# Kernel tuning notes

Measured on AMD Instinct MI355X. Metric: run time of the kernel, lower is better.

Reference implementation:

```python
import jax, jax.numpy as jnp
import numpy as np

B, N, D_IN = 8, 8192, 13
RATIO, R, K = 0.25, 0.2, 32


def setup_inputs() -> dict:
    key = jax.random.key(0)
    k1, k2, k3, k4 = jax.random.split(key, 4)
    x = jax.random.normal(k1, (B, N, D_IN), dtype=jnp.float32)
    pos = jax.random.uniform(k2, (B, N, 3), dtype=jnp.float32)
    batch = jnp.broadcast_to(jnp.arange(B, dtype=jnp.int32)[:, None], (B, N))
    W1 = jax.random.normal(k3, (D_IN + 3, 64), dtype=jnp.float32) * 0.1
    b1 = jnp.zeros((64,), jnp.float32)
    W2 = jax.random.normal(k4, (64, 128), dtype=jnp.float32) * 0.1
    b2 = jnp.zeros((128,), jnp.float32)
    return {"x": x, "pos": pos, "batch": batch, "W1": W1, "b1": b1, "W2": W2, "b2": b2}


def _fps_single(p, M):
    """Deterministic farthest point sampling (start at index 0). p: [N,3] -> [M] int32."""
    n = p.shape[0]

    def step(carry, _):
        mind, last = carry
        d = jnp.sum((p - p[last]) ** 2, axis=-1)
        mind = jnp.minimum(mind, d)
        nxt = jnp.argmax(mind).astype(jnp.int32)
        return (mind, nxt), nxt

    init = (jnp.full((n,), 1e10, p.dtype), jnp.int32(0))
    _, rest = jax.lax.scan(step, init, None, length=M - 1)
    return jnp.concatenate([jnp.zeros((1,), jnp.int32), rest])


def reference(x, pos, batch, W1, b1, W2, b2):
    M = int(RATIO * N)
    # --- FPS per cloud ---
    idx = jax.vmap(lambda p: _fps_single(p, M))(pos)              # [B, M]
    pos_s = jnp.take_along_axis(pos, idx[..., None], axis=1)      # [B, M, 3]
    # --- radius ball query: first K in-ball neighbors by point index ---
    d2 = jnp.sum((pos_s[:, :, None, :] - pos[:, None, :, :]) ** 2, axis=-1)  # [B, M, N]
    within = d2 <= R * R
    rank = jnp.where(within, jnp.arange(N, dtype=jnp.int32), N)   # invalid -> N
    negv, nbr = jax.lax.top_k(-rank, K)                           # K smallest ranks
    valid = negv > -N                                             # [B, M, K]
    # --- gather -> local_nn MLP -> masked max-scatter (PointNetConv) ---
    x_j = jax.vmap(lambda a, i: a[i])(x, nbr)                     # [B, M, K, D_IN]
    pos_j = jax.vmap(lambda a, i: a[i])(pos, nbr)                 # [B, M, K, 3]
    feat = jnp.concatenate([x_j, pos_j - pos_s[:, :, None, :]], axis=-1)
    h = jax.nn.relu(feat @ W1 + b1)
    h = jax.nn.relu(h @ W2 + b2)                                  # [B, M, K, 128]
    h = jnp.where(valid[..., None], h, -jnp.inf)
    x_out = jnp.max(h, axis=2)                                    # [B, M, 128]
    batch_s = jnp.take_along_axis(batch, idx, axis=1)             # [B, M]
    return x_out, pos_s, batch_s
```

## Files before the change

### kernel.cpp

```cpp
#include <hip/hip_runtime.h>
#include <cstddef>

#define B_   8
#define N_   8192
#define M_   2048
#define K_   32
#define DIN_ 13

typedef _Float16 f16x8 __attribute__((ext_vector_type(8)));
typedef float    f32x4 __attribute__((ext_vector_type(4)));

template <int CTRL>
__device__ __forceinline__ float dppmax(float v) {
  int o = __builtin_amdgcn_update_dpp(
      (int)0xff800000, __float_as_int(v), CTRL, 0xF, 0xF, false);
  return fmaxf(v, __int_as_float(o));
}
template <int CTRL>
__device__ __forceinline__ unsigned dppminu(unsigned v) {
  unsigned o = (unsigned)__builtin_amdgcn_update_dpp(
      (int)0xFFFFFFFF, (int)v, CTRL, 0xF, 0xF, false);
  return v < o ? v : o;
}
__device__ __forceinline__ float wave_reduce_max(float v) {
  v = dppmax<0x111>(v); v = dppmax<0x112>(v); v = dppmax<0x114>(v);
  v = dppmax<0x118>(v); v = dppmax<0x142>(v); v = dppmax<0x143>(v);
  return __int_as_float(__builtin_amdgcn_readlane(__float_as_int(v), 63));
}
__device__ __forceinline__ unsigned wave_reduce_min_u32(unsigned v) {
  v = dppminu<0x111>(v); v = dppminu<0x112>(v); v = dppminu<0x114>(v);
  v = dppminu<0x118>(v); v = dppminu<0x142>(v); v = dppminu<0x143>(v);
  return (unsigned)__builtin_amdgcn_readlane((int)v, 63);
}

__global__ __launch_bounds__(1024, 4) void fps_kernel(
    const float* __restrict__ pos,
    float* __restrict__ pos_s,
    float* __restrict__ batch_s)
{
  const int b    = blockIdx.x;
  const int t    = threadIdx.x;
  const int lane = t & 63;
  const int wid  = t >> 6;
  const float* p = pos + (size_t)b * N_ * 3;

  __shared__ float px_l[N_], py_l[N_], pz_l[N_];
  __shared__ int   r2o[N_];
  __shared__ int   vbase[512];
  __shared__ int   vcur[512];
  __shared__ int   wsum[8];
  __shared__ unsigned long long kslot[3];

  for (int mm = t; mm < M_; mm += 1024)
    batch_s[b * M_ + mm] = (float)b;
  if (t < 512) vcur[t] = 0;
  if (t == 0) { kslot[0] = 0ull; kslot[1] = 0ull; kslot[2] = 0ull; }
  __syncthreads();

  int vid[8];
#pragma unroll
  for (int i = 0; i < 8; ++i) {
    int j = t + 1024 * i;
    float x = p[j * 3 + 0], y = p[j * 3 + 1], z = p[j * 3 + 2];
    px_l[j] = x; py_l[j] = y; pz_l[j] = z;
    int ix = (int)(x * 8.f); ix = ix < 0 ? 0 : (ix > 7 ? 7 : ix);
    int iy = (int)(y * 8.f); iy = iy < 0 ? 0 : (iy > 7 ? 7 : iy);
    int iz = (int)(z * 8.f); iz = iz < 0 ? 0 : (iz > 7 ? 7 : iz);
    int v = (ix & 1) | ((iy & 1) << 1) | ((iz & 1) << 2) |
            (((ix >> 1) & 1) << 3) | (((iy >> 1) & 1) << 4) |
            (((iz >> 1) & 1) << 5) |
            ((ix >> 2) << 6) | ((iy >> 2) << 7) | ((iz >> 2) << 8);
    vid[i] = v;
    atomicAdd(&vcur[v], 1);
  }
  __syncthreads();

  int h = 0, sc = 0;
  if (t < 512) {
    h = vcur[t]; sc = h;
#pragma unroll
    for (int d = 1; d < 64; d <<= 1) {
      int o = __shfl_up(sc, d);
      if (lane >= d) sc += o;
    }
    if (lane == 63) wsum[wid] = sc;
  }
  __syncthreads();
  if (t < 8) {
    int v = wsum[t]; int inc = v;
#pragma unroll
    for (int d = 1; d < 8; d <<= 1) {
      int o = __shfl_up(inc, d);
      if (t >= d) inc += o;
    }
    wsum[t] = inc - v;
  }
  __syncthreads();
  if (t < 512) { vbase[t] = sc - h + wsum[t >> 6]; vcur[t] = 0; }
  __syncthreads();

#pragma unroll
  for (int i = 0; i < 8; ++i) {
    int j = t + 1024 * i;
    int r = vbase[vid[i]] + atomicAdd(&vcur[vid[i]], 1);
    r2o[r] = j;
  }
  __syncthreads();

  float px[8], py[8], pz[8], mind[8]; int oi[8];
#pragma unroll
  for (int i = 0; i < 8; ++i) {
    int o = r2o[t * 8 + i];
    oi[i] = o;
    px[i] = px_l[o]; py[i] = py_l[o]; pz[i] = pz_l[o];
    mind[i] = 1e10f;
  }
#pragma unroll
  for (int i = 0; i < 8; ++i) {
    asm volatile("" : "+v"(px[i]), "+v"(py[i]), "+v"(pz[i]));
  }

  float bxmin = px[0], bxmax = px[0], bymin = py[0], bymax = py[0],
        bzmin = pz[0], bzmax = pz[0];
#pragma unroll
  for (int i = 1; i < 8; ++i) {
    bxmin = fminf(bxmin, px[i]); bxmax = fmaxf(bxmax, px[i]);
    bymin = fminf(bymin, py[i]); bymax = fmaxf(bymax, py[i]);
    bzmin = fminf(bzmin, pz[i]); bzmax = fmaxf(bzmax, pz[i]);
  }

  float lx = px_l[0], ly = py_l[0], lz = pz_l[0];
  if (t == 0) {
    pos_s[(size_t)b * M_ * 3 + 0] = lx;
    pos_s[(size_t)b * M_ * 3 + 1] = ly;
    pos_s[(size_t)b * M_ * 3 + 2] = lz;
  }

  float ltm = 1e10f;
  float cwm = 0.f;
  unsigned cmin = 0xFFFFFFFFu;
  int sl = 1;
  int rs = 0;

  for (int s = 1; s < M_; ++s) {
    float cx = fmaxf(fmaxf(bxmin - lx, lx - bxmax), 0.f);
    float cy = fmaxf(fmaxf(bymin - ly, ly - bymax), 0.f);
    float cz = fmaxf(fmaxf(bzmin - lz, lz - bzmax), 0.f);
    float LB = (cx * cx + cy * cy) + cz * cz;
    bool lp = (LB * 0.999999f < ltm);
    if (__ballot(lp) != 0ull) {
      float tmax;
      {
#pragma clang fp contract(off)
#pragma unroll
        for (int i = 0; i < 8; ++i) {
          float dx = px[i] - lx, dy = py[i] - ly, dz = pz[i] - lz;
          float d  = (dx * dx + dy * dy) + dz * dz;
          mind[i]  = fminf(mind[i], d);
        }
        float m0 = fmaxf(mind[0], mind[1]), m1 = fmaxf(mind[2], mind[3]);
        float m2 = fmaxf(mind[4], mind[5]), m3 = fmaxf(mind[6], mind[7]);
        tmax = fmaxf(fmaxf(m0, m1), fmaxf(m2, m3));
      }
      ltm = tmax;
      const float wm = wave_reduce_max(tmax);
      unsigned cc = 0xFFFFFFFFu;
#pragma unroll
      for (int i = 0; i < 8; ++i) {
        unsigned cand = (mind[i] == wm) ? (unsigned)oi[i] : 0xFFFFFFFFu;
        cc = cc < cand ? cc : cand;
      }
      cmin = wave_reduce_min_u32(cc);
      cwm = wm;
    }
    if (lane == 0) {
      unsigned long long key =
          ((unsigned long long)__float_as_uint(cwm) << 32) |
          (unsigned long long)(0xFFFFFFFFu - cmin);
      atomicMax(&kslot[sl], key);
    }
    __syncthreads();
    if (t == 0) kslot[rs] = 0ull;
    const unsigned long long kk = kslot[sl];
    const int wj  = (int)(0xFFFFFFFFu - (unsigned int)(kk & 0xFFFFFFFFull));
    const int wju = (int)__builtin_amdgcn_readfirstlane(wj);
    lx = px_l[wju]; ly = py_l[wju]; lz = pz_l[wju];
    if (t == 0) {
      size_t o2 = ((size_t)b * M_ + s) * 3;
      pos_s[o2 + 0] = lx; pos_s[o2 + 1] = ly; pos_s[o2 + 2] = lz;
    }
    sl = (sl == 2) ? 0 : sl + 1;
    rs = (rs == 2) ? 0 : rs + 1;
  }
}

__global__ __launch_bounds__(256) void prep_kernel(
    const float* __restrict__ W1, const float* __restrict__ W2,
    _Float16* __restrict__ w1t, _Float16* __restrict__ w2t)
{
  int t = blockIdx.x * 256 + threadIdx.x;
  if (t < 8192) {
    int n = t >> 6, k = t & 63;
    w2t[t] = (_Float16)W2[k * 128 + n];
  }
  int u = t - 8192;
  if (u >= 0 && u < 1024) {
    int n = u >> 4, k = u & 15;
    w1t[u] = (_Float16)W1[k * 64 + n];
  }
}

__global__ __launch_bounds__(64) void sa_kernel(
    const float* __restrict__ x,
    const float* __restrict__ pos,
    const float* __restrict__ b1,
    const float* __restrict__ b2,
    const float* __restrict__ pos_s,
    const _Float16* __restrict__ w1t,
    const _Float16* __restrict__ w2t,
    float* __restrict__ x_out)
{
  const int blk  = blockIdx.x;
  const int b    = blk >> 11;
  const int m    = blk & 2047;
  const int lane = threadIdx.x;
  const int l15  = lane & 15;
  const int quad = lane >> 4;

  __shared__ int      nbr[K_];
  __shared__ _Float16 featb[K_][24];
  __shared__ _Float16 h1b[K_][72];

  const float* pb = pos + (size_t)b * N_ * 3;
  const float* xb = x   + (size_t)b * N_ * DIN_;
  const size_t so = ((size_t)b * M_ + m) * 3;
  const float sx = pos_s[so + 0];
  const float sy = pos_s[so + 1];
  const float sz = pos_s[so + 2];
  const float R2 = (float)(0.2 * 0.2);

  int cnt = 0;
  for (int base = 0; base < N_ && cnt < K_; base += 64) {
    int j = base + lane;
    float qx = pb[j * 3 + 0], qy = pb[j * 3 + 1], qz = pb[j * 3 + 2];
    bool win;
    {
#pragma clang fp contract(off)
      float dx = sx - qx, dy = sy - qy, dz = sz - qz;
      float d2 = (dx * dx + dy * dy) + dz * dz;
      win = d2 <= R2;
    }
    unsigned long long mk = __ballot(win);
    int rank = (int)__popcll(mk & ((1ull << lane) - 1ull));
    if (win) {
      int slot = cnt + rank;
      if (slot < K_) nbr[slot] = j;
    }
    cnt += (int)__popcll(mk);
  }
  const int valid = cnt < K_ ? cnt : K_;
  __syncthreads();

  for (int tq = lane; tq < K_ * 16; tq += 64) {
    int r = tq >> 4, i = tq & 15;
    float v = 0.f;
    if (r < valid) {
      int j = nbr[r];
      if (i < DIN_) {
        v = xb[j * DIN_ + i];
      } else {
        float c = (i == 13) ? sx : (i == 14) ? sy : sz;
        float q = pb[j * 3 + (i - 13)];
        v = q - c;
      }
    }
    featb[r][i] = (_Float16)v;
  }
  __syncthreads();

  f16x8 fz;
#pragma unroll
  for (int i = 0; i < 8; ++i) fz[i] = (_Float16)0;

  f16x8 a1[2], b1f[4];
#pragma unroll
  for (int mt = 0; mt < 2; ++mt)
    a1[mt] = (quad < 2) ? *(const f16x8*)&featb[mt * 16 + l15][quad * 8] : fz;
#pragma unroll
  for (int nt = 0; nt < 4; ++nt)
    b1f[nt] = (quad < 2) ? *(const f16x8*)&w1t[(nt * 16 + l15) * 16 + quad * 8]
                         : fz;

#pragma unroll
  for (int mt = 0; mt < 2; ++mt) {
#pragma unroll
    for (int nt = 0; nt < 4; ++nt) {
      f32x4 c = {0.f, 0.f, 0.f, 0.f};
      c = __builtin_amdgcn_mfma_f32_16x16x32_f16(a1[mt], b1f[nt], c, 0, 0, 0);
      float bb = b1[nt * 16 + l15];
#pragma unroll
      for (int r = 0; r < 4; ++r) {
        float v = c[r] + bb;
        h1b[mt * 16 + quad * 4 + r][nt * 16 + l15] =
            (_Float16)(v > 0.f ? v : 0.f);
      }
    }
  }
  __syncthreads();

  f16x8 a2[2][2];
#pragma unroll
  for (int mt = 0; mt < 2; ++mt)
#pragma unroll
    for (int kt = 0; kt < 2; ++kt)
      a2[mt][kt] = *(const f16x8*)&h1b[mt * 16 + l15][kt * 32 + quad * 8];

  float* o = x_out + ((size_t)b * M_ + m) * 128;
#pragma unroll
  for (int nt = 0; nt < 8; ++nt) {
    f16x8 b20 = *(const f16x8*)&w2t[(nt * 16 + l15) * 64 + 0 * 32 + quad * 8];
    f16x8 b21 = *(const f16x8*)&w2t[(nt * 16 + l15) * 64 + 1 * 32 + quad * 8];
    f32x4 c0 = {0.f, 0.f, 0.f, 0.f}, c1 = {0.f, 0.f, 0.f, 0.f};
    c0 = __builtin_amdgcn_mfma_f32_16x16x32_f16(a2[0][0], b20, c0, 0, 0, 0);
    c0 = __builtin_amdgcn_mfma_f32_16x16x32_f16(a2[0][1], b21, c0, 0, 0, 0);
    c1 = __builtin_amdgcn_mfma_f32_16x16x32_f16(a2[1][0], b20, c1, 0, 0, 0);
    c1 = __builtin_amdgcn_mfma_f32_16x16x32_f16(a2[1][1], b21, c1, 0, 0, 0);
    float bv = b2[nt * 16 + l15];
    float acc = -INFINITY;
#pragma unroll
    for (int r = 0; r < 4; ++r) {
      int row0 = quad * 4 + r;
      int row1 = 16 + quad * 4 + r;
      float v0 = c0[r] + bv; v0 = v0 > 0.f ? v0 : 0.f;
      float v1 = c1[r] + bv; v1 = v1 > 0.f ? v1 : 0.f;
      if (row0 < valid) acc = fmaxf(acc, v0);
      if (row1 < valid) acc = fmaxf(acc, v1);
    }
    acc = fmaxf(acc, __shfl_xor(acc, 16));
    acc = fmaxf(acc, __shfl_xor(acc, 32));
    if (quad == 0) o[nt * 16 + l15] = acc;
  }
}

extern "C" void kernel_launch(void* const* d_in, const int* in_sizes, int n_in,
                              void* d_out, int out_size, void* d_ws, size_t ws_size,
                              hipStream_t stream) {
  (void)in_sizes; (void)n_in; (void)ws_size; (void)out_size;
  const float* x   = (const float*)d_in[0];
  const float* pos = (const float*)d_in[1];
  const float* W1  = (const float*)d_in[3];
  const float* b1  = (const float*)d_in[4];
  const float* W2  = (const float*)d_in[5];
  const float* b2  = (const float*)d_in[6];

  float* out     = (float*)d_out;
  float* x_out   = out;
  float* pos_s   = out + (size_t)B_ * M_ * 128;
  float* batch_s = pos_s + (size_t)B_ * M_ * 3;

  _Float16* w1t = (_Float16*)d_ws;
  _Float16* w2t = w1t + 1024;

  prep_kernel<<<36, 256, 0, stream>>>(W1, W2, w1t, w2t);
  fps_kernel<<<B_, 1024, 0, stream>>>(pos, pos_s, batch_s);
  sa_kernel<<<B_ * M_, 64, 0, stream>>>(x, pos, b1, b2, pos_s, w1t, w2t, x_out);
}
```

Measured before the change: 1.504 ms.

## Fuse FPS and set-abstraction into one cooperative kernel with progress-flag overlap

Merges the farthest-point-sampling kernel and the per-centroid MLP kernel into a single cooperative launch. Eight blocks run FPS and publish a per-cloud progress counter every 32 samples, while 240 worker blocks of 16 waves spin-wait on that counter and process centroids as soon as they are available. The goal is to hide the SA work behind the long serial FPS loop instead of running it afterwards. In exchange it relies on co-residency from the cooperative launch, spin-polling with sleeps, and wave-level LDS syncs in place of block barriers.

```diff
diff --git a/kernel.cpp b/kernel.cpp
--- a/kernel.cpp
+++ b/kernel.cpp
@@ -6,6 +6,8 @@
 #define M_   2048
 #define K_   32
 #define DIN_ 13
+#define NWRK 240
+#define NBLK (8 + NWRK)
 
 typedef _Float16 f16x8 __attribute__((ext_vector_type(8)));
 typedef float    f32x4 __attribute__((ext_vector_type(4)));
@@ -33,203 +35,40 @@
   return (unsigned)__builtin_amdgcn_readlane((int)v, 63);
 }
 
-__global__ __launch_bounds__(1024, 4) void fps_kernel(
-    const float* __restrict__ pos,
-    float* __restrict__ pos_s,
-    float* __restrict__ batch_s)
+#define WAVE_LDS_SYNC()                                   \
+  do {                                                    \
+    asm volatile("s_waitcnt lgkmcnt(0)" ::: "memory");    \
+    __builtin_amdgcn_wave_barrier();                      \
+  } while (0)
+
+struct FpsLds {
+  float px[N_], py[N_], pz[N_];
+  int   r2o[N_];
+  int   vbase[512];
+  int   vcur[512];
+  int   wsum[8];
+  unsigned long long kslot[3];
+};
+struct __align__(16) SaSlice {
+  int      nbr[K_];
+  _Float16 featb[K_][24];
+  _Float16 h1b[K_][72];
+};
+union SmemU {
+  FpsLds  fps;
+  SaSlice sa[16];
+};
+
+__device__ __forceinline__ void sa_wave(
+    int b, int m, int lane,
+    const float* __restrict__ x, const float* __restrict__ pos,
+    const float* __restrict__ b1, const float* __restrict__ b2,
+    const float* __restrict__ pos_s,
+    const _Float16* __restrict__ w1t, const _Float16* __restrict__ w2t,
+    float* __restrict__ x_out, SaSlice* sl)
 {
-  const int b    = blockIdx.x;
-  const int t    = threadIdx.x;
-  const int lane = t & 63;
-  const int wid  = t >> 6;
-  const float* p = pos + (size_t)b * N_ * 3;
-
-  __shared__ float px_l[N_], py_l[N_], pz_l[N_];
-  __shared__ int   r2o[N_];
-  __shared__ int   vbase[512];
-  __shared__ int   vcur[512];
-  __shared__ int   wsum[8];
-  __shared__ unsigned long long kslot[3];
-
-  for (int mm = t; mm < M_; mm += 1024)
-    batch_s[b * M_ + mm] = (float)b;
-  if (t < 512) vcur[t] = 0;
-  if (t == 0) { kslot[0] = 0ull; kslot[1] = 0ull; kslot[2] = 0ull; }
-  __syncthreads();
-
-  int vid[8];
-#pragma unroll
-  for (int i = 0; i < 8; ++i) {
-    int j = t + 1024 * i;
-    float x = p[j * 3 + 0], y = p[j * 3 + 1], z = p[j * 3 + 2];
-    px_l[j] = x; py_l[j] = y; pz_l[j] = z;
-    int ix = (int)(x * 8.f); ix = ix < 0 ? 0 : (ix > 7 ? 7 : ix);
-    int iy = (int)(y * 8.f); iy = iy < 0 ? 0 : (iy > 7 ? 7 : iy);
-    int iz = (int)(z * 8.f); iz = iz < 0 ? 0 : (iz > 7 ? 7 : iz);
-    int v = (ix & 1) | ((iy & 1) << 1) | ((iz & 1) << 2) |
-            (((ix >> 1) & 1) << 3) | (((iy >> 1) & 1) << 4) |
-            (((iz >> 1) & 1) << 5) |
-            ((ix >> 2) << 6) | ((iy >> 2) << 7) | ((iz >> 2) << 8);
-    vid[i] = v;
-    atomicAdd(&vcur[v], 1);
-  }
-  __syncthreads();
-
-  int h = 0, sc = 0;
-  if (t < 512) {
-    h = vcur[t]; sc = h;
-#pragma unroll
-    for (int d = 1; d < 64; d <<= 1) {
-      int o = __shfl_up(sc, d);
-      if (lane >= d) sc += o;
-    }
-    if (lane == 63) wsum[wid] = sc;
-  }
-  __syncthreads();
-  if (t < 8) {
-    int v = wsum[t]; int inc = v;
-#pragma unroll
-    for (int d = 1; d < 8; d <<= 1) {
-      int o = __shfl_up(inc, d);
-      if (t >= d) inc += o;
-    }
-    wsum[t] = inc - v;
-  }
-  __syncthreads();
-  if (t < 512) { vbase[t] = sc - h + wsum[t >> 6]; vcur[t] = 0; }
-  __syncthreads();
-
-#pragma unroll
-  for (int i = 0; i < 8; ++i) {
-    int j = t + 1024 * i;
-    int r = vbase[vid[i]] + atomicAdd(&vcur[vid[i]], 1);
-    r2o[r] = j;
-  }
-  __syncthreads();
-
-  float px[8], py[8], pz[8], mind[8]; int oi[8];
-#pragma unroll
-  for (int i = 0; i < 8; ++i) {
-    int o = r2o[t * 8 + i];
-    oi[i] = o;
-    px[i] = px_l[o]; py[i] = py_l[o]; pz[i] = pz_l[o];
-    mind[i] = 1e10f;
-  }
-#pragma unroll
-  for (int i = 0; i < 8; ++i) {
-    asm volatile("" : "+v"(px[i]), "+v"(py[i]), "+v"(pz[i]));
-  }
-
-  float bxmin = px[0], bxmax = px[0], bymin = py[0], bymax = py[0],
-        bzmin = pz[0], bzmax = pz[0];
-#pragma unroll
-  for (int i = 1; i < 8; ++i) {
-    bxmin = fminf(bxmin, px[i]); bxmax = fmaxf(bxmax, px[i]);
-    bymin = fminf(bymin, py[i]); bymax = fmaxf(bymax, py[i]);
-    bzmin = fminf(bzmin, pz[i]); bzmax = fmaxf(bzmax, pz[i]);
-  }
-
-  float lx = px_l[0], ly = py_l[0], lz = pz_l[0];
-  if (t == 0) {
-    pos_s[(size_t)b * M_ * 3 + 0] = lx;
-    pos_s[(size_t)b * M_ * 3 + 1] = ly;
-    pos_s[(size_t)b * M_ * 3 + 2] = lz;
-  }
-
-  float ltm = 1e10f;
-  float cwm = 0.f;
-  unsigned cmin = 0xFFFFFFFFu;
-  int sl = 1;
-  int rs = 0;
-
-  for (int s = 1; s < M_; ++s) {
-    float cx = fmaxf(fmaxf(bxmin - lx, lx - bxmax), 0.f);
-    float cy = fmaxf(fmaxf(bymin - ly, ly - bymax), 0.f);
-    float cz = fmaxf(fmaxf(bzmin - lz, lz - bzmax), 0.f);
-    float LB = (cx * cx + cy * cy) + cz * cz;
-    bool lp = (LB * 0.999999f < ltm);
-    if (__ballot(lp) != 0ull) {
-      float tmax;
-      {
-#pragma clang fp contract(off)
-#pragma unroll
-        for (int i = 0; i < 8; ++i) {
-          float dx = px[i] - lx, dy = py[i] - ly, dz = pz[i] - lz;
-          float d  = (dx * dx + dy * dy) + dz * dz;
-          mind[i]  = fminf(mind[i], d);
-        }
-        float m0 = fmaxf(mind[0], mind[1]), m1 = fmaxf(mind[2], mind[3]);
-        float m2 = fmaxf(mind[4], mind[5]), m3 = fmaxf(mind[6], mind[7]);
-        tmax = fmaxf(fmaxf(m0, m1), fmaxf(m2, m3));
-      }
-      ltm = tmax;
-      const float wm = wave_reduce_max(tmax);
-      unsigned cc = 0xFFFFFFFFu;
-#pragma unroll
-      for (int i = 0; i < 8; ++i) {
-        unsigned cand = (mind[i] == wm) ? (unsigned)oi[i] : 0xFFFFFFFFu;
-        cc = cc < cand ? cc : cand;
-      }
-      cmin = wave_reduce_min_u32(cc);
-      cwm = wm;
-    }
-    if (lane == 0) {
-      unsigned long long key =
-          ((unsigned long long)__float_as_uint(cwm) << 32) |
-          (unsigned long long)(0xFFFFFFFFu - cmin);
-      atomicMax(&kslot[sl], key);
-    }
-    __syncthreads();
-    if (t == 0) kslot[rs] = 0ull;
-    const unsigned long long kk = kslot[sl];
-    const int wj  = (int)(0xFFFFFFFFu - (unsigned int)(kk & 0xFFFFFFFFull));
-    const int wju = (int)__builtin_amdgcn_readfirstlane(wj);
-    lx = px_l[wju]; ly = py_l[wju]; lz = pz_l[wju];
-    if (t == 0) {
-      size_t o2 = ((size_t)b * M_ + s) * 3;
-      pos_s[o2 + 0] = lx; pos_s[o2 + 1] = ly; pos_s[o2 + 2] = lz;
-    }
-    sl = (sl == 2) ? 0 : sl + 1;
-    rs = (rs == 2) ? 0 : rs + 1;
-  }
-}
-
-__global__ __launch_bounds__(256) void prep_kernel(
-    const float* __restrict__ W1, const float* __restrict__ W2,
-    _Float16* __restrict__ w1t, _Float16* __restrict__ w2t)
-{
-  int t = blockIdx.x * 256 + threadIdx.x;
-  if (t < 8192) {
-    int n = t >> 6, k = t & 63;
-    w2t[t] = (_Float16)W2[k * 128 + n];
-  }
-  int u = t - 8192;
-  if (u >= 0 && u < 1024) {
-    int n = u >> 4, k = u & 15;
-    w1t[u] = (_Float16)W1[k * 64 + n];
-  }
-}
-
-__global__ __launch_bounds__(64) void sa_kernel(
-    const float* __restrict__ x,
-    const float* __restrict__ pos,
-    const float* __restrict__ b1,
-    const float* __restrict__ b2,
-    const float* __restrict__ pos_s,
-    const _Float16* __restrict__ w1t,
-    const _Float16* __restrict__ w2t,
-    float* __restrict__ x_out)
-{
-  const int blk  = blockIdx.x;
-  const int b    = blk >> 11;
-  const int m    = blk & 2047;
-  const int lane = threadIdx.x;
   const int l15  = lane & 15;
   const int quad = lane >> 4;
-
-  __shared__ int      nbr[K_];
-  __shared__ _Float16 featb[K_][24];
-  __shared__ _Float16 h1b[K_][72];
 
   const float* pb = pos + (size_t)b * N_ * 3;
   const float* xb = x   + (size_t)b * N_ * DIN_;
@@ -254,18 +93,18 @@
     int rank = (int)__popcll(mk & ((1ull << lane) - 1ull));
     if (win) {
       int slot = cnt + rank;
-      if (slot < K_) nbr[slot] = j;
+      if (slot < K_) sl->nbr[slot] = j;
     }
     cnt += (int)__popcll(mk);
   }
   const int valid = cnt < K_ ? cnt : K_;
-  __syncthreads();
+  WAVE_LDS_SYNC();
 
   for (int tq = lane; tq < K_ * 16; tq += 64) {
     int r = tq >> 4, i = tq & 15;
     float v = 0.f;
     if (r < valid) {
-      int j = nbr[r];
+      int j = sl->nbr[r];
       if (i < DIN_) {
         v = xb[j * DIN_ + i];
       } else {
@@ -274,9 +113,9 @@
         v = q - c;
       }
     }
-    featb[r][i] = (_Float16)v;
-  }
-  __syncthreads();
+    sl->featb[r][i] = (_Float16)v;
+  }
+  WAVE_LDS_SYNC();
 
   f16x8 fz;
 #pragma unroll
@@ -285,7 +124,8 @@
   f16x8 a1[2], b1f[4];
 #pragma unroll
   for (int mt = 0; mt < 2; ++mt)
-    a1[mt] = (quad < 2) ? *(const f16x8*)&featb[mt * 16 + l15][quad * 8] : fz;
+    a1[mt] = (quad < 2) ? *(const f16x8*)&sl->featb[mt * 16 + l15][quad * 8]
+                        : fz;
 #pragma unroll
   for (int nt = 0; nt < 4; ++nt)
     b1f[nt] = (quad < 2) ? *(const f16x8*)&w1t[(nt * 16 + l15) * 16 + quad * 8]
@@ -301,19 +141,19 @@
 #pragma unroll
       for (int r = 0; r < 4; ++r) {
         float v = c[r] + bb;
-        h1b[mt * 16 + quad * 4 + r][nt * 16 + l15] =
+        sl->h1b[mt * 16 + quad * 4 + r][nt * 16 + l15] =
             (_Float16)(v > 0.f ? v : 0.f);
       }
     }
   }
-  __syncthreads();
+  WAVE_LDS_SYNC();
 
   f16x8 a2[2][2];
 #pragma unroll
   for (int mt = 0; mt < 2; ++mt)
 #pragma unroll
     for (int kt = 0; kt < 2; ++kt)
-      a2[mt][kt] = *(const f16x8*)&h1b[mt * 16 + l15][kt * 32 + quad * 8];
+      a2[mt][kt] = *(const f16x8*)&sl->h1b[mt * 16 + l15][kt * 32 + quad * 8];
 
   float* o = x_out + ((size_t)b * M_ + m) * 128;
 #pragma unroll
@@ -342,6 +182,202 @@
   }
 }
 
+__global__ __launch_bounds__(1024, 4) void fused_kernel(
+    const float* __restrict__ x, const float* __restrict__ pos,
+    const float* __restrict__ b1, const float* __restrict__ b2,
+    const _Float16* __restrict__ w1t, const _Float16* __restrict__ w2t,
+    float* __restrict__ pos_s, float* __restrict__ batch_s,
+    float* __restrict__ x_out, int* __restrict__ progress)
+{
+  __shared__ SmemU u;
+  const int t    = threadIdx.x;
+  const int lane = t & 63;
+  const int wid  = t >> 6;
+
+  if (blockIdx.x < 8) {
+    const int b = blockIdx.x;
+    const float* p = pos + (size_t)b * N_ * 3;
+
+    for (int mm = t; mm < M_; mm += 1024)
+      batch_s[b * M_ + mm] = (float)b;
+    if (t < 512) u.fps.vcur[t] = 0;
+    if (t == 0) { u.fps.kslot[0] = 0ull; u.fps.kslot[1] = 0ull;
+                  u.fps.kslot[2] = 0ull; }
+    __syncthreads();
+
+    int vid[8];
+#pragma unroll
+    for (int i = 0; i < 8; ++i) {
+      int j = t + 1024 * i;
+      float xx = p[j * 3 + 0], yy = p[j * 3 + 1], zz = p[j * 3 + 2];
+      u.fps.px[j] = xx; u.fps.py[j] = yy; u.fps.pz[j] = zz;
+      int ix = (int)(xx * 8.f); ix = ix < 0 ? 0 : (ix > 7 ? 7 : ix);
+      int iy = (int)(yy * 8.f); iy = iy < 0 ? 0 : (iy > 7 ? 7 : iy);
+      int iz = (int)(zz * 8.f); iz = iz < 0 ? 0 : (iz > 7 ? 7 : iz);
+      int v = (ix & 1) | ((iy & 1) << 1) | ((iz & 1) << 2) |
+              (((ix >> 1) & 1) << 3) | (((iy >> 1) & 1) << 4) |
+              (((iz >> 1) & 1) << 5) |
+              ((ix >> 2) << 6) | ((iy >> 2) << 7) | ((iz >> 2) << 8);
+      vid[i] = v;
+      atomicAdd(&u.fps.vcur[v], 1);
+    }
+    __syncthreads();
+
+    int h = 0, sc = 0;
+    if (t < 512) {
+      h = u.fps.vcur[t]; sc = h;
+#pragma unroll
+      for (int d = 1; d < 64; d <<= 1) {
+        int o = __shfl_up(sc, d);
+        if (lane >= d) sc += o;
+      }
+      if (lane == 63) u.fps.wsum[wid] = sc;
+    }
+    __syncthreads();
+    if (t < 8) {
+      int v = u.fps.wsum[t]; int inc = v;
+#pragma unroll
+      for (int d = 1; d < 8; d <<= 1) {
+        int o = __shfl_up(inc, d);
+        if (t >= d) inc += o;
+      }
+      u.fps.wsum[t] = inc - v;
+    }
+    __syncthreads();
+    if (t < 512) { u.fps.vbase[t] = sc - h + u.fps.wsum[t >> 6];
+                   u.fps.vcur[t] = 0; }
+    __syncthreads();
+
+#pragma unroll
+    for (int i = 0; i < 8; ++i) {
+      int j = t + 1024 * i;
+      int r = u.fps.vbase[vid[i]] + atomicAdd(&u.fps.vcur[vid[i]], 1);
+      u.fps.r2o[r] = j;
+    }
+    __syncthreads();
+
+    float px[8], py[8], pz[8], mind[8]; int oi[8];
+#pragma unroll
+    for (int i = 0; i < 8; ++i) {
+      int o = u.fps.r2o[t * 8 + i];
+      oi[i] = o;
+      px[i] = u.fps.px[o]; py[i] = u.fps.py[o]; pz[i] = u.fps.pz[o];
+      mind[i] = 1e10f;
+    }
+#pragma unroll
+    for (int i = 0; i < 8; ++i) {
+      asm volatile("" : "+v"(px[i]), "+v"(py[i]), "+v"(pz[i]));
+    }
+
+    float bxmin = px[0], bxmax = px[0], bymin = py[0], bymax = py[0],
+          bzmin = pz[0], bzmax = pz[0];
+#pragma unroll
+    for (int i = 1; i < 8; ++i) {
+      bxmin = fminf(bxmin, px[i]); bxmax = fmaxf(bxmax, px[i]);
+      bymin = fminf(bymin, py[i]); bymax = fmaxf(bymax, py[i]);
+      bzmin = fminf(bzmin, pz[i]); bzmax = fmaxf(bzmax, pz[i]);
+    }
+
+    float lx = u.fps.px[0], ly = u.fps.py[0], lz = u.fps.pz[0];
+    if (t == 0) {
+      pos_s[(size_t)b * M_ * 3 + 0] = lx;
+      pos_s[(size_t)b * M_ * 3 + 1] = ly;
+      pos_s[(size_t)b * M_ * 3 + 2] = lz;
+    }
+
+    float ltm = 1e10f;
+    float cwm = 0.f;
+    unsigned cmin = 0xFFFFFFFFu;
+    int slm = 1;
+    int rsm = 0;
+
+    for (int s = 1; s < M_; ++s) {
+      float cx = fmaxf(fmaxf(bxmin - lx, lx - bxmax), 0.f);
+      float cy = fmaxf(fmaxf(bymin - ly, ly - bymax), 0.f);
+      float cz = fmaxf(fmaxf(bzmin - lz, lz - bzmax), 0.f);
+      float LB = (cx * cx + cy * cy) + cz * cz;
+      bool lp = (LB * 0.999999f < ltm);
+      if (__ballot(lp) != 0ull) {
+        float tmax;
+        {
+#pragma clang fp contract(off)
+#pragma unroll
+          for (int i = 0; i < 8; ++i) {
+            float dx = px[i] - lx, dy = py[i] - ly, dz = pz[i] - lz;
+            float d  = (dx * dx + dy * dy) + dz * dz;
+            mind[i]  = fminf(mind[i], d);
+          }
+          float m0 = fmaxf(mind[0], mind[1]), m1 = fmaxf(mind[2], mind[3]);
+          float m2 = fmaxf(mind[4], mind[5]), m3 = fmaxf(mind[6], mind[7]);
+          tmax = fmaxf(fmaxf(m0, m1), fmaxf(m2, m3));
+        }
+        ltm = tmax;
+        const float wm = wave_reduce_max(tmax);
+        unsigned cc = 0xFFFFFFFFu;
+#pragma unroll
+        for (int i = 0; i < 8; ++i) {
+          unsigned cand = (mind[i] == wm) ? (unsigned)oi[i] : 0xFFFFFFFFu;
+          cc = cc < cand ? cc : cand;
+        }
+        cmin = wave_reduce_min_u32(cc);
+        cwm = wm;
+      }
+      if (lane == 0) {
+        unsigned long long key =
+            ((unsigned long long)__float_as_uint(cwm) << 32) |
+            (unsigned long long)(0xFFFFFFFFu - cmin);
+        atomicMax(&u.fps.kslot[slm], key);
+      }
+      __syncthreads();
+      if (t == 0) u.fps.kslot[rsm] = 0ull;
+      const unsigned long long kk = u.fps.kslot[slm];
+      const int wj  = (int)(0xFFFFFFFFu - (unsigned int)(kk & 0xFFFFFFFFull));
+      const int wju = (int)__builtin_amdgcn_readfirstlane(wj);
+      lx = u.fps.px[wju]; ly = u.fps.py[wju]; lz = u.fps.pz[wju];
+      if (t == 0) {
+        size_t o2 = ((size_t)b * M_ + s) * 3;
+        pos_s[o2 + 0] = lx; pos_s[o2 + 1] = ly; pos_s[o2 + 2] = lz;
+        if ((s & 31) == 31)
+          __hip_atomic_store(&progress[b], s + 1, __ATOMIC_RELEASE,
+                             __HIP_MEMORY_SCOPE_AGENT);
+      }
+      slm = (slm == 2) ? 0 : slm + 1;
+      rsm = (rsm == 2) ? 0 : rsm + 1;
+    }
+  } else {
+    SaSlice* sl = &u.sa[wid];
+    const int wgw = (blockIdx.x - 8) * 16 + wid;
+    for (int task = wgw; task < B_ * M_; task += NWRK * 16) {
+      const int b = task >> 11, m = task & (M_ - 1);
+      if (lane == 0) {
+        while (__hip_atomic_load(&progress[b], __ATOMIC_RELAXED,
+                                 __HIP_MEMORY_SCOPE_AGENT) <= m)
+          __builtin_amdgcn_s_sleep(10);
+      }
+      __threadfence();
+      sa_wave(b, m, lane, x, pos, b1, b2, pos_s, w1t, w2t, x_out, sl);
+    }
+  }
+}
+
+__global__ __launch_bounds__(256) void prep_kernel(
+    const float* __restrict__ W1, const float* __restrict__ W2,
+    _Float16* __restrict__ w1t, _Float16* __restrict__ w2t,
+    int* __restrict__ progress)
+{
+  int t = blockIdx.x * 256 + threadIdx.x;
+  if (t < 8192) {
+    int n = t >> 6, k = t & 63;
+    w2t[t] = (_Float16)W2[k * 128 + n];
+  }
+  int u = t - 8192;
+  if (u >= 0 && u < 1024) {
+    int n = u >> 4, k = u & 15;
+    w1t[u] = (_Float16)W1[k * 64 + n];
+  }
+  if (blockIdx.x == 0 && threadIdx.x < 8) progress[threadIdx.x] = 0;
+}
+
 extern "C" void kernel_launch(void* const* d_in, const int* in_sizes, int n_in,
                               void* d_out, int out_size, void* d_ws, size_t ws_size,
                               hipStream_t stream) {
@@ -360,8 +396,14 @@
 
   _Float16* w1t = (_Float16*)d_ws;
   _Float16* w2t = w1t + 1024;
-
-  prep_kernel<<<36, 256, 0, stream>>>(W1, W2, w1t, w2t);
-  fps_kernel<<<B_, 1024, 0, stream>>>(pos, pos_s, batch_s);
-  sa_kernel<<<B_ * M_, 64, 0, stream>>>(x, pos, b1, b2, pos_s, w1t, w2t, x_out);
-}
+  int* progress = (int*)(w2t + 8192);
+
+  prep_kernel<<<36, 256, 0, stream>>>(W1, W2, w1t, w2t, progress);
+
+  void* kargs[] = {
+      (void*)&x, (void*)&pos, (void*)&b1, (void*)&b2,
+      (void*)&w1t, (void*)&w2t, (void*)&pos_s, (void*)&batch_s,
+      (void*)&x_out, (void*)&progress};
+  hipLaunchCooperativeKernel((const void*)fused_kernel,
+                             dim3(NBLK), dim3(1024), kargs, 0, stream);
+}
```

New measurement: 1.533 ms. About the same (+1.9%).
